# Optimization experiments

Hardware: AMD Instinct MI355X
Metric: run time of the kernel (lower is better)

Reference implementation:

```python
import jax, jax.numpy as jnp
import numpy as np

NV, NC, E, H, L = 100_000, 420_000, 630_000, 128, 8
ALPHA, THETA = 0.1, 0.5


def _seg_mean(msgs, dst, n_dst):
    # mean aggregation over destination segments (PyG SAGEConv default)
    s = jax.ops.segment_sum(msgs, dst, num_segments=n_dst)
    cnt = jax.ops.segment_sum(jnp.ones((dst.shape[0], 1), msgs.dtype), dst, num_segments=n_dst)
    return s / jnp.maximum(cnt, 1.0)


def _sage(x_src, x_dst, src, dst, n_dst, Wl, bl, Wr):
    # SAGEConv: lin_l(mean_{j in N(i)} x_j) + lin_r(x_i); lin_r has no bias
    agg = _seg_mean(x_src[src], dst, n_dst)
    return agg @ Wl + bl + x_dst @ Wr


def setup_inputs() -> dict:
    key = jax.random.key(0)
    ks = jax.random.split(key, 40)
    k = iter(range(40))
    rn = lambda shape, s=0.05: jax.random.normal(ks[next(k)], shape, jnp.float32) * s
    inp = {}
    inp['x_variable'] = jax.random.normal(ks[next(k)], (NV, 4), jnp.float32)
    inp['x_clause'] = jax.random.normal(ks[next(k)], (NC, 1), jnp.float32)
    src_p = jax.random.randint(ks[next(k)], (E,), 0, NV)
    dst_p = jax.random.randint(ks[next(k)], (E,), 0, NC)
    src_n = jax.random.randint(ks[next(k)], (E,), 0, NV)
    dst_n = jax.random.randint(ks[next(k)], (E,), 0, NC)
    inp['edge_pos'] = jnp.stack([src_p, dst_p])  # variable -> clause
    inp['edge_neg'] = jnp.stack([src_n, dst_n])
    inp['W_vemb'] = rn((4, H)); inp['b_vemb'] = rn((H,))
    inp['W_cemb'] = rn((1, H)); inp['b_cemb'] = rn((H,))
    for tag in ('pos', 'neg', 'rpos', 'rneg'):
        inp[f'Wl_{tag}'] = rn((L, H, H)); inp[f'bl_{tag}'] = rn((L, H))
        inp[f'Wr_{tag}'] = rn((L, H, H))
    inp['Wv'] = rn((L, H, H)); inp['bv'] = rn((L, H))
    inp['W_fin'] = rn((H, 1)); inp['b_fin'] = rn((1,))
    return inp


def reference(x_variable, x_clause, edge_pos, edge_neg,
              W_vemb, b_vemb, W_cemb, b_cemb,
              Wl_pos, bl_pos, Wr_pos, Wl_neg, bl_neg, Wr_neg,
              Wl_rpos, bl_rpos, Wr_rpos, Wl_rneg, bl_rneg, Wr_rneg,
              Wv, bv, W_fin, b_fin):
    v_h0 = jax.nn.relu(x_variable @ W_vemb + b_vemb)
    c_h0 = jax.nn.relu(x_clause @ W_cemb + b_cemb)
    v_h, c_h = v_h0, c_h0
    sp, dp = edge_pos[0], edge_pos[1]
    sn, dn = edge_neg[0], edge_neg[1]
    for i in range(L):
        v_old = v_h
        # HeteroConv(aggr='sum'): clause gets pos_in + neg_in, variable gets rev_pos_in + rev_neg_in
        c_new = (_sage(v_h, c_h, sp, dp, NC, Wl_pos[i], bl_pos[i], Wr_pos[i]) +
                 _sage(v_h, c_h, sn, dn, NC, Wl_neg[i], bl_neg[i], Wr_neg[i]))
        v_new = (_sage(c_h, v_h, dp, sp, NV, Wl_rpos[i], bl_rpos[i], Wr_rpos[i]) +
                 _sage(c_h, v_h, dn, sn, NV, Wl_rneg[i], bl_rneg[i], Wr_rneg[i]))
        v_h = (1.0 - ALPHA) * v_new + ALPHA * v_h0
        c_h = (1.0 - ALPHA) * c_new + ALPHA * c_h0
        beta = float(np.log(THETA / (i + 1) + 1.0))
        v_h = (1.0 - beta) * v_h + beta * (v_h @ Wv[i] + bv[i])
        v_h = v_h + v_old  # use_inter_layer_res=True
        v_h, c_h = jax.nn.relu(v_h), jax.nn.relu(c_h)
    return v_h @ W_fin + b_fin
```

## Files before the change

### kernel.cpp

```cpp
#include <hip/hip_runtime.h>
#include <math.h>

#define NVV 100000
#define NCC 420000
#define EE  630000
#define HH  128
#define LL  8

typedef unsigned int uint;
typedef unsigned short ushort;
typedef __attribute__((ext_vector_type(8))) short bf16x8;
typedef __attribute__((ext_vector_type(4))) float f32x4;

#define MFMA16(a,b,c) __builtin_amdgcn_mfma_f32_16x16x32_bf16(a,b,c,0,0,0)
#define SW(r,k) (((r)<<7) + ((k) ^ (((r)&7)<<3)))

__device__ inline float bf2f(uint u){ return __uint_as_float(u << 16); }
__device__ inline uint  f2bf(float f){
  uint b = __float_as_uint(f);
  return (b + 0x7FFFu + ((b >> 16) & 1u)) >> 16;
}
__device__ inline uint pack2(float a, float b){ return f2bf(a) | (f2bf(b) << 16); }
__device__ inline float4 relu4(float4 v){
  v.x = fmaxf(v.x, 0.f); v.y = fmaxf(v.y, 0.f);
  v.z = fmaxf(v.z, 0.f); v.w = fmaxf(v.w, 0.f);
  return v;
}

__global__ void k_sentinel(float* out, float v){
  if (blockIdx.x == 0 && threadIdx.x == 0) out[0] = v;
}

__device__ inline float4 vemb4(const float* __restrict__ xv, const float* __restrict__ W,
                               const float* __restrict__ b, int i, int h4){
  float x0 = xv[4*i+0], x1 = xv[4*i+1], x2 = xv[4*i+2], x3 = xv[4*i+3];
  float4 w0 = *(const float4*)(W + 0*HH + h4);
  float4 w1 = *(const float4*)(W + 1*HH + h4);
  float4 w2 = *(const float4*)(W + 2*HH + h4);
  float4 w3 = *(const float4*)(W + 3*HH + h4);
  float4 bb = *(const float4*)(b + h4);
  float4 r;
  r.x = fmaf(x0,w0.x, fmaf(x1,w1.x, fmaf(x2,w2.x, fmaf(x3,w3.x, bb.x))));
  r.y = fmaf(x0,w0.y, fmaf(x1,w1.y, fmaf(x2,w2.y, fmaf(x3,w3.y, bb.y))));
  r.z = fmaf(x0,w0.z, fmaf(x1,w1.z, fmaf(x2,w2.z, fmaf(x3,w3.z, bb.z))));
  r.w = fmaf(x0,w0.w, fmaf(x1,w1.w, fmaf(x2,w2.w, fmaf(x3,w3.w, bb.w))));
  return r;
}

__global__ void k_embed_v(const float* __restrict__ xv, const float* __restrict__ W,
                          const float* __restrict__ b, float* __restrict__ out){
  int tid = blockIdx.x * 256 + threadIdx.x;
  int i = tid >> 5;
  if (i >= NVV) return;
  int h4 = (tid & 31) << 2;
  *(float4*)(out + (size_t)i*HH + h4) = relu4(vemb4(xv, W, b, i, h4));
}

__global__ void k_embed_c(const float* __restrict__ xc, const float* __restrict__ W,
                          const float* __restrict__ b, uint* __restrict__ out){
  int tid = blockIdx.x * 256 + threadIdx.x;
  int i = tid >> 5;
  if (i >= NCC) return;
  int c2 = tid & 31;
  int h4 = c2 << 2;
  float x0 = xc[i];
  float4 w = *(const float4*)(W + h4);
  float4 bb = *(const float4*)(b + h4);
  float4 r;
  r.x = fmaxf(fmaf(x0, w.x, bb.x), 0.f);
  r.y = fmaxf(fmaf(x0, w.y, bb.y), 0.f);
  r.z = fmaxf(fmaf(x0, w.z, bb.z), 0.f);
  r.w = fmaxf(fmaf(x0, w.w, bb.w), 0.f);
  uint2 o; o.x = pack2(r.x, r.y); o.y = pack2(r.z, r.w);
  *(uint2*)(out + (size_t)i*64 + c2*2) = o;
}

__global__ void k_prep(const float* __restrict__ Wl_pos, const float* __restrict__ Wl_neg,
                       const float* __restrict__ Wl_rpos, const float* __restrict__ Wl_rneg,
                       const float* __restrict__ Wv, const float* __restrict__ Wr_pos,
                       const float* __restrict__ Wr_neg, const float* __restrict__ Wr_rpos,
                       const float* __restrict__ Wr_rneg, ushort* __restrict__ wt){
  int tid = blockIdx.x * 256 + threadIdx.x;
  int n4 = tid & 31, k = (tid >> 5) & 127, l = (tid >> 12) & 7, m = tid >> 15;
  const float* s1; const float* s2 = nullptr;
  switch (m){
    case 0: s1 = Wl_pos;  break;
    case 1: s1 = Wl_neg;  break;
    case 2: s1 = Wl_rpos; break;
    case 3: s1 = Wl_rneg; break;
    case 4: s1 = Wv;      break;
    case 5: s1 = Wr_pos;  s2 = Wr_neg;  break;
    default: s1 = Wr_rpos; s2 = Wr_rneg; break;
  }
  size_t o = (size_t)l*16384 + (size_t)k*128 + n4*4;
  float4 w = *(const float4*)(s1 + o);
  if (s2){
    float4 w2 = *(const float4*)(s2 + o);
    w.x += w2.x; w.y += w2.y; w.z += w2.z; w.w += w2.w;
  }
  ushort* hi = wt + (size_t)((m*LL + l)*2    )*16384;
  ushort* lo = wt + (size_t)((m*LL + l)*2 + 1)*16384;
  float vv[4] = {w.x, w.y, w.z, w.w};
  #pragma unroll
  for (int e = 0; e < 4; ++e){
    int n = n4*4 + e;
    uint h = f2bf(vv[e]);
    float r = vv[e] - bf2f(h);
    hi[SW(n, k)] = (ushort)h;
    lo[SW(n, k)] = (ushort)f2bf(r);
  }
}

__global__ void k_counti(const int* __restrict__ d, int* cnt, int n){
  int i = blockIdx.x * 256 + threadIdx.x;
  if (i < n) atomicAdd(&cnt[d[i]], 1);
}

#define SCAN256(ts, t) \
  for (int off = 1; off < 256; off <<= 1){ \
    int _a = (t >= off) ? ts[t - off] : 0; \
    __syncthreads(); \
    ts[t] += _a; \
    __syncthreads(); \
  }

__global__ void k_scanb(const int* __restrict__ in, int* __restrict__ out,
                        int* __restrict__ part, int n){
  __shared__ int ts[256];
  int b = blockIdx.x, t = threadIdx.x;
  int base = b*1024 + t*4;
  int v0 = (base+0 < n) ? in[base+0] : 0;
  int v1 = (base+1 < n) ? in[base+1] : 0;
  int v2 = (base+2 < n) ? in[base+2] : 0;
  int v3 = (base+3 < n) ? in[base+3] : 0;
  int s1 = v0, s2 = s1+v1, s3 = s2+v2, tsum = s3+v3;
  ts[t] = tsum; __syncthreads();
  SCAN256(ts, t)
  int excl = ts[t] - tsum;
  if (base+0 < n) out[base+0] = excl;
  if (base+1 < n) out[base+1] = excl + s1;
  if (base+2 < n) out[base+2] = excl + s2;
  if (base+3 < n) out[base+3] = excl + s3;
  if (t == 255) part[b] = ts[255];
}

__global__ void k_scanp(int* p, int nb){
  __shared__ int ts[256];
  __shared__ int carry;
  int t = threadIdx.x;
  if (t == 0) carry = 0;
  __syncthreads();
  for (int c = 0; c*256 < nb; ++c){
    int i = c*256 + t;
    int v = (i < nb) ? p[i] : 0;
    ts[t] = v; __syncthreads();
    SCAN256(ts, t)
    int excl = ts[t] - v + carry;
    if (i < nb) p[i] = excl;
    int tot = ts[255];
    __syncthreads();
    if (t == 0) carry += tot;
    __syncthreads();
  }
}

__global__ void k_scana(int* out, const int* __restrict__ part, int n){
  int i = blockIdx.x * 256 + threadIdx.x;
  if (i < n) out[i] += part[i >> 10];
}

__global__ void k_fill(const int* __restrict__ dst, const int* __restrict__ pay,
                       int* cur, int* __restrict__ eo, int n){
  int i = blockIdx.x * 256 + threadIdx.x;
  if (i >= n) return;
  int p = atomicAdd(&cur[dst[i]], 1);
  eo[p] = pay[i];
}

__global__ void k_vgather(const uint* __restrict__ ch,
                          const int* __restrict__ ipp, const int* __restrict__ epp,
                          const int* __restrict__ ipn, const int* __restrict__ epn,
                          uint* __restrict__ Up, uint* __restrict__ Un){
  int g = blockIdx.x * 256 + threadIdx.x;
  int v = g >> 6, lane = g & 63;
  if (v >= NVV) return;
  int sp = v ? ipp[v-1] : 0, ePos = ipp[v];
  int sn = v ? ipn[v-1] : 0, eNeg = ipn[v];
  float p0 = 0.f, p1 = 0.f, n0 = 0.f, n1 = 0.f;
  int jp = sp, jn = sn;
  while (jp < ePos && jn < eNeg){
    uint up = ch[(size_t)epp[jp]*64 + lane];
    uint un = ch[(size_t)epn[jn]*64 + lane];
    p0 += bf2f(up & 0xFFFFu); p1 += bf2f(up >> 16);
    n0 += bf2f(un & 0xFFFFu); n1 += bf2f(un >> 16);
    ++jp; ++jn;
  }
  for (; jp < ePos; ++jp){
    uint up = ch[(size_t)epp[jp]*64 + lane];
    p0 += bf2f(up & 0xFFFFu); p1 += bf2f(up >> 16);
  }
  for (; jn < eNeg; ++jn){
    uint un = ch[(size_t)epn[jn]*64 + lane];
    n0 += bf2f(un & 0xFFFFu); n1 += bf2f(un >> 16);
  }
  float ivp = 1.f / fmaxf((float)(ePos - sp), 1.f);
  float ivn = 1.f / fmaxf((float)(eNeg - sn), 1.f);
  Up[(size_t)v*64 + lane] = pack2(p0*ivp, p1*ivp);
  Un[(size_t)v*64 + lane] = pack2(n0*ivn, n1*ivn);
}

__device__ inline void stA_bf16(const uint4* __restrict__ A, ushort* As, int m0, int M, int t){
  #pragma unroll
  for (int j = 0; j < 4; ++j){
    int idx = j*512 + t, r = idx >> 4, c = idx & 15;
    uint4 v = make_uint4(0,0,0,0);
    if (m0 + r < M) v = A[(size_t)(m0 + r)*16 + c];
    *(uint4*)(As + SW(r, c*8)) = v;
  }
}

__device__ inline void stA_f32(const float* __restrict__ A, ushort* As, int m0, int M, int t){
  const float4* A4 = (const float4*)A;
  #pragma unroll
  for (int j = 0; j < 8; ++j){
    int idx = j*512 + t, r = idx >> 5, c = idx & 31;
    float4 v = make_float4(0.f,0.f,0.f,0.f);
    if (m0 + r < M) v = A4[(size_t)(m0 + r)*32 + c];
    uint2 u; u.x = pack2(v.x, v.y); u.y = pack2(v.z, v.w);
    *(uint2*)(As + SW(r, c*4)) = u;
  }
}

__device__ inline void stB(const uint4* __restrict__ Bt, ushort* Bs, int t){
  #pragma unroll
  for (int j = 0; j < 4; ++j) ((uint4*)Bs)[j*512 + t] = Bt[j*512 + t];
}

__device__ inline void kloop(const ushort* As, const ushort* Bs, int wr, int wc,
                             int l15, int g, f32x4 acc[2][4]){
  #pragma unroll
  for (int kk = 0; kk < 4; ++kk){
    int kb = kk*32 + g*8;
    bf16x8 a0 = *(const bf16x8*)(As + SW(wr*32 + l15,      kb));
    bf16x8 a1 = *(const bf16x8*)(As + SW(wr*32 + 16 + l15, kb));
    #pragma unroll
    for (int ni = 0; ni < 4; ++ni){
      int n = wc*64 + ni*16 + l15;
      bf16x8 b = *(const bf16x8*)(Bs + SW(n, kb));
      acc[0][ni] = MFMA16(a0, b, acc[0][ni]);
      acc[1][ni] = MFMA16(a1, b, acc[1][ni]);
    }
  }
}

__device__ inline void accStoreF(float* ldsF, f32x4 acc[2][4], int wr, int wc, int l15, int g){
  #pragma unroll
  for (int mi = 0; mi < 2; ++mi)
    #pragma unroll
    for (int ni = 0; ni < 4; ++ni)
      #pragma unroll
      for (int j = 0; j < 4; ++j)
        ldsF[(wr*32 + mi*16 + g*4 + j)*128 + wc*64 + ni*16 + l15] = acc[mi][ni][j];
}

__device__ inline void accStoreFsw(float* ldsF, f32x4 acc[2][4], int wr, int wc, int l15, int g){
  #pragma unroll
  for (int mi = 0; mi < 2; ++mi)
    #pragma unroll
    for (int ni = 0; ni < 4; ++ni)
      #pragma unroll
      for (int j = 0; j < 4; ++j){
        int r = wr*32 + mi*16 + g*4 + j;
        int c = wc*64 + ni*16 + l15;
        ldsF[r*128 + (((c >> 2) ^ (r & 31)) << 2) + (c & 3)] = acc[mi][ni][j];
      }
}

__device__ inline void accStoreBf(ushort* dst, f32x4 acc[2][4], int wr, int wc, int l15, int g){
  #pragma unroll
  for (int mi = 0; mi < 2; ++mi)
    #pragma unroll
    for (int ni = 0; ni < 4; ++ni)
      #pragma unroll
      for (int j = 0; j < 4; ++j)
        dst[(wr*32 + mi*16 + g*4 + j)*128 + wc*64 + ni*16 + l15] =
            (ushort)f2bf(acc[mi][ni][j]);
}

#define MMHEAD \
  __shared__ ushort lds[32768]; \
  ushort* As = lds; ushort* Bs = lds + 16384; \
  float* accumF = (float*)lds; \
  int t = threadIdx.x, m0 = blockIdx.x * 128; \
  int w = t >> 6, l = t & 63, wr = w >> 1, wc = w & 1, l15 = l & 15, g = l >> 4; \
  const f32x4 zz = {0.f, 0.f, 0.f, 0.f}; \
  (void)accumF;

#define ZACC(A) { \
  _Pragma("unroll") for (int mi_ = 0; mi_ < 2; ++mi_) \
    _Pragma("unroll") for (int ni_ = 0; ni_ < 4; ++ni_) A[mi_][ni_] = zz; }

__global__ __launch_bounds__(512) void k_fused_v(
    const uint4* __restrict__ AggP, const uint4* __restrict__ AggN,
    const uint4* __restrict__ Bph, const uint4* __restrict__ Bpl,
    const uint4* __restrict__ Bnh, const uint4* __restrict__ Bnl,
    const uint4* __restrict__ Bfh, const uint4* __restrict__ Bfl,
    const uint4* __restrict__ Byph, const uint4* __restrict__ Bypl,
    const uint4* __restrict__ Bynh, const uint4* __restrict__ Bynl,
    const uint4* __restrict__ Bvh, const uint4* __restrict__ Bvl,
    const float* __restrict__ xv, const float* __restrict__ Wve, const float* __restrict__ bve,
    const float* __restrict__ blp, const float* __restrict__ bln, const float* __restrict__ bvv,
    float omb, float beta,
    uint4* __restrict__ Yp, uint4* __restrict__ Yn, float* vh, int M){
  MMHEAD
  f32x4 accM[2][4], accP[2][4], accN[2][4];
  ZACC(accM) ZACC(accP) ZACC(accN)

  stA_bf16(AggP, As, m0, M, t); stB(Bph, Bs, t); __syncthreads();
  kloop(As, Bs, wr, wc, l15, g, accM); __syncthreads();
  stB(Bpl, Bs, t); __syncthreads();
  kloop(As, Bs, wr, wc, l15, g, accM); __syncthreads();
  stA_bf16(AggN, As, m0, M, t); stB(Bnh, Bs, t); __syncthreads();
  kloop(As, Bs, wr, wc, l15, g, accM); __syncthreads();
  stB(Bnl, Bs, t); __syncthreads();
  kloop(As, Bs, wr, wc, l15, g, accM); __syncthreads();
  stA_f32(vh, As, m0, M, t); stB(Bfh, Bs, t); __syncthreads();
  kloop(As, Bs, wr, wc, l15, g, accM); __syncthreads();
  stB(Bfl, Bs, t); __syncthreads();
  kloop(As, Bs, wr, wc, l15, g, accM); __syncthreads();
  stB(Byph, Bs, t); __syncthreads();
  kloop(As, Bs, wr, wc, l15, g, accP); __syncthreads();
  stB(Bypl, Bs, t); __syncthreads();
  kloop(As, Bs, wr, wc, l15, g, accP); __syncthreads();
  stB(Bynh, Bs, t); __syncthreads();
  kloop(As, Bs, wr, wc, l15, g, accN); __syncthreads();
  stB(Bynl, Bs, t); __syncthreads();
  kloop(As, Bs, wr, wc, l15, g, accN); __syncthreads();

  accStoreBf(lds,         accP, wr, wc, l15, g);
  accStoreBf(lds + 16384, accN, wr, wc, l15, g);
  __syncthreads();
  #pragma unroll
  for (int j = 0; j < 4; ++j){
    int idx = j*512 + t, r = idx >> 4, c = idx & 15;
    if (m0 + r < M){
      Yp[(size_t)(m0 + r)*16 + c] = ((const uint4*)lds)[idx];
      Yn[(size_t)(m0 + r)*16 + c] = ((const uint4*)(lds + 16384))[idx];
    }
  }
  __syncthreads();

  accStoreF(accumF, accM, wr, wc, l15, g);
  __syncthreads();
  float4 vreg[8];
  #pragma unroll
  for (int j = 0; j < 8; ++j){
    int idx = j*512 + t, r = idx >> 5, c4 = idx & 31;
    int row = m0 + r;
    float4 o = make_float4(0.f,0.f,0.f,0.f);
    if (row < M){
      float4 a4 = ((const float4*)accumF)[r*32 + c4];
      float4 bp = ((const float4*)blp)[c4];
      float4 bn = ((const float4*)bln)[c4];
      float4 h = relu4(vemb4(xv, Wve, bve, row, c4*4));
      o.x = 0.9f*(a4.x + bp.x + bn.x) + 0.1f*h.x;
      o.y = 0.9f*(a4.y + bp.y + bn.y) + 0.1f*h.y;
      o.z = 0.9f*(a4.z + bp.z + bn.z) + 0.1f*h.z;
      o.w = 0.9f*(a4.w + bp.w + bn.w) + 0.1f*h.w;
    }
    vreg[j] = o;
  }
  __syncthreads();
  #pragma unroll
  for (int j = 0; j < 8; ++j){
    int idx = j*512 + t, r = idx >> 5, c4 = idx & 31;
    uint2 u; u.x = pack2(vreg[j].x, vreg[j].y); u.y = pack2(vreg[j].z, vreg[j].w);
    *(uint2*)(As + SW(r, c4*4)) = u;
  }
  f32x4 accT[2][4];
  ZACC(accT)
  stB(Bvh, Bs, t); __syncthreads();
  kloop(As, Bs, wr, wc, l15, g, accT); __syncthreads();
  stB(Bvl, Bs, t); __syncthreads();
  kloop(As, Bs, wr, wc, l15, g, accT);

  float* ldsH = (float*)Bs;
  #pragma unroll
  for (int half = 0; half < 2; ++half){
    __syncthreads();
    if ((wr >> 1) == half){
      int rbase = (wr & 1)*32;
      #pragma unroll
      for (int mi = 0; mi < 2; ++mi)
        #pragma unroll
        for (int ni = 0; ni < 4; ++ni)
          #pragma unroll
          for (int j = 0; j < 4; ++j)
            ldsH[(rbase + mi*16 + g*4 + j)*128 + wc*64 + ni*16 + l15] = accT[mi][ni][j];
    }
    __syncthreads();
    #pragma unroll
    for (int j = 0; j < 4; ++j){
      int idx = j*512 + t, r2 = idx >> 5, c4 = idx & 31;
      int row = m0 + half*64 + r2;
      if (row >= M) continue;
      float4 a4 = ((const float4*)ldsH)[r2*32 + c4];
      uint2 um = *(const uint2*)(As + SW(half*64 + r2, c4*4));
      float4 bb = ((const float4*)bvv)[c4];
      float4 vo = *(const float4*)(vh + (size_t)row*HH + c4*4);
      float m0f = bf2f(um.x & 0xFFFFu), m1f = bf2f(um.x >> 16);
      float m2f = bf2f(um.y & 0xFFFFu), m3f = bf2f(um.y >> 16);
      float4 o;
      o.x = fmaxf(omb*m0f + beta*(a4.x + bb.x) + vo.x, 0.f);
      o.y = fmaxf(omb*m1f + beta*(a4.y + bb.y) + vo.y, 0.f);
      o.z = fmaxf(omb*m2f + beta*(a4.z + bb.z) + vo.z, 0.f);
      o.w = fmaxf(omb*m3f + beta*(a4.w + bb.w) + vo.w, 0.f);
      *(float4*)(vh + (size_t)row*HH + c4*4) = o;
    }
  }
}

__device__ inline void addrow8(float f[8], uint4 u){
  f[0] += bf2f(u.x & 0xFFFFu); f[1] += bf2f(u.x >> 16);
  f[2] += bf2f(u.y & 0xFFFFu); f[3] += bf2f(u.y >> 16);
  f[4] += bf2f(u.z & 0xFFFFu); f[5] += bf2f(u.z >> 16);
  f[6] += bf2f(u.w & 0xFFFFu); f[7] += bf2f(u.w >> 16);
}

__global__ __launch_bounds__(512) void k_mm_c(const uint4* ch,
    const uint4* __restrict__ Bh, const uint4* __restrict__ Bl,
    const int* __restrict__ ipp, const int* __restrict__ ecp,
    const int* __restrict__ ipn, const int* __restrict__ ecn,
    const uint4* __restrict__ Yp, const uint4* __restrict__ Yn,
    const float* __restrict__ xc, const float* __restrict__ Wc, const float* __restrict__ bc,
    const float* __restrict__ blp, const float* __restrict__ bln,
    uint4* chout){
  MMHEAD
  f32x4 acc[2][4];
  ZACC(acc)
  stA_bf16(ch, As, m0, NCC, t); stB(Bh, Bs, t); __syncthreads();
  kloop(As, Bs, wr, wc, l15, g, acc); __syncthreads();
  stB(Bl, Bs, t); __syncthreads();
  kloop(As, Bs, wr, wc, l15, g, acc); __syncthreads();
  accStoreFsw(accumF, acc, wr, wc, l15, g);
  __syncthreads();

  int c16 = t & 15;
  int rg  = t >> 4;
  #pragma unroll
  for (int pass = 0; pass < 4; ++pass){
    int r = pass*32 + rg;
    int row = m0 + r;
    if (row >= NCC) continue;
    float fp[8] = {0,0,0,0,0,0,0,0};
    float fn[8] = {0,0,0,0,0,0,0,0};
    int sp = row ? ipp[row-1] : 0, ePos = ipp[row];
    int sn = row ? ipn[row-1] : 0, eNeg = ipn[row];
    int jp = sp, jn = sn;
    while (jp < ePos && jn < eNeg){
      uint4 up = Yp[(size_t)ecp[jp]*16 + c16];
      uint4 un = Yn[(size_t)ecn[jn]*16 + c16];
      addrow8(fp, up);
      addrow8(fn, un);
      ++jp; ++jn;
    }
    for (; jp < ePos; ++jp) addrow8(fp, Yp[(size_t)ecp[jp]*16 + c16]);
    for (; jn < eNeg; ++jn) addrow8(fn, Yn[(size_t)ecn[jn]*16 + c16]);
    float invp = 1.f / fmaxf((float)(ePos - sp), 1.f);
    float invn = 1.f / fmaxf((float)(eNeg - sn), 1.f);

    int gi0 = c16*2, gi1 = gi0 + 1;
    float4 res0 = ((const float4*)accumF)[r*32 + (gi0 ^ (r & 31))];
    float4 res1 = ((const float4*)accumF)[r*32 + (gi1 ^ (r & 31))];
    float4 wc0 = ((const float4*)Wc)[gi0],  wc1 = ((const float4*)Wc)[gi1];
    float4 bc0 = ((const float4*)bc)[gi0],  bc1 = ((const float4*)bc)[gi1];
    float4 bp0 = ((const float4*)blp)[gi0], bp1 = ((const float4*)blp)[gi1];
    float4 bn0 = ((const float4*)bln)[gi0], bn1 = ((const float4*)bln)[gi1];
    float xcv = xc[row];
    float res[8] = {res0.x,res0.y,res0.z,res0.w, res1.x,res1.y,res1.z,res1.w};
    float wcv[8] = {wc0.x,wc0.y,wc0.z,wc0.w, wc1.x,wc1.y,wc1.z,wc1.w};
    float bcv[8] = {bc0.x,bc0.y,bc0.z,bc0.w, bc1.x,bc1.y,bc1.z,bc1.w};
    float bpv[8] = {bp0.x,bp0.y,bp0.z,bp0.w, bp1.x,bp1.y,bp1.z,bp1.w};
    float bnv[8] = {bn0.x,bn0.y,bn0.z,bn0.w, bn1.x,bn1.y,bn1.z,bn1.w};
    float o[8];
    #pragma unroll
    for (int k = 0; k < 8; ++k){
      float h = fmaxf(fmaf(xcv, wcv[k], bcv[k]), 0.f);
      float m = fmaf(fp[k], invp, fn[k]*invn);
      o[k] = fmaxf(0.9f*(m + res[k] + bpv[k] + bnv[k]) + 0.1f*h, 0.f);
    }
    uint4 u;
    u.x = pack2(o[0], o[1]); u.y = pack2(o[2], o[3]);
    u.z = pack2(o[4], o[5]); u.w = pack2(o[6], o[7]);
    chout[(size_t)row*16 + c16] = u;
  }
}

__global__ void k_final(const float* __restrict__ vh, const float* __restrict__ wf,
                        const float* __restrict__ bf, float* __restrict__ out){
  int wid = (blockIdx.x * 256 + threadIdx.x) >> 6;
  if (wid >= NVV) return;
  int lane = threadIdx.x & 63;
  float2 a = *(const float2*)(vh + (size_t)wid*HH + lane*2);
  float2 w = *(const float2*)(wf + lane*2);
  float s = a.x*w.x + a.y*w.y;
  #pragma unroll
  for (int off = 32; off > 0; off >>= 1) s += __shfl_down(s, off);
  if (lane == 0) out[wid] = s + bf[0];
}

extern "C" void kernel_launch(void* const* d_in, const int* in_sizes, int n_in,
                              void* d_out, int out_size, void* d_ws, size_t ws_size,
                              hipStream_t stream) {
  const float* xv  = (const float*)d_in[0];
  const float* xc  = (const float*)d_in[1];
  const int*   ep  = (const int*)d_in[2];
  const int*   en  = (const int*)d_in[3];
  const float* Wve = (const float*)d_in[4];
  const float* bve = (const float*)d_in[5];
  const float* Wce = (const float*)d_in[6];
  const float* bce = (const float*)d_in[7];
  const float* Wl_pos  = (const float*)d_in[8];
  const float* bl_pos  = (const float*)d_in[9];
  const float* Wr_pos  = (const float*)d_in[10];
  const float* Wl_neg  = (const float*)d_in[11];
  const float* bl_neg  = (const float*)d_in[12];
  const float* Wr_neg  = (const float*)d_in[13];
  const float* Wl_rpos = (const float*)d_in[14];
  const float* bl_rpos = (const float*)d_in[15];
  const float* Wr_rpos = (const float*)d_in[16];
  const float* Wl_rneg = (const float*)d_in[17];
  const float* bl_rneg = (const float*)d_in[18];
  const float* Wr_rneg = (const float*)d_in[19];
  const float* Wv  = (const float*)d_in[20];
  const float* bv  = (const float*)d_in[21];
  const float* Wf  = (const float*)d_in[22];
  const float* bf  = (const float*)d_in[23];
  float* out = (float*)d_out;

  size_t off = 0;
  auto alloc = [&](size_t bytes) -> void* {
    void* p = (char*)d_ws + off;
    off = (off + bytes + 255) & ~(size_t)255;
    return p;
  };
  uint*   c_h  = (uint*)  alloc((size_t)NCC*64*sizeof(uint));
  float*  v_h  = (float*) alloc((size_t)NVV*HH*sizeof(float));
  uint*   U1   = (uint*)  alloc((size_t)NVV*64*sizeof(uint));
  uint*   U2   = (uint*)  alloc((size_t)NVV*64*sizeof(uint));
  ushort* wt   = (ushort*)alloc((size_t)7*LL*2*16384*sizeof(ushort));
  int*   ipc_p = (int*)  alloc((size_t)NCC*sizeof(int));
  int*   ec_p  = (int*)  alloc((size_t)EE*sizeof(int));
  int*   ipc_n = (int*)  alloc((size_t)NCC*sizeof(int));
  int*   ec_n  = (int*)  alloc((size_t)EE*sizeof(int));
  int*   ipv_p = (int*)  alloc((size_t)NVV*sizeof(int));
  int*   ev_p  = (int*)  alloc((size_t)EE*sizeof(int));
  int*   ipv_n = (int*)  alloc((size_t)NVV*sizeof(int));
  int*   ev_n  = (int*)  alloc((size_t)EE*sizeof(int));
  int*   part  = (int*)  alloc(4096);
  if (off > ws_size){
    k_sentinel<<<1, 64, 0, stream>>>(out, (float)(ws_size >> 20));
    return;
  }

  const int TB = 256;
  const int gE  = (EE + TB-1)/TB;
  const int gV  = (NVV*32 + TB-1)/TB;
  const int gC  = (NCC*32 + TB-1)/TB;
  const int gGv = (NVV + 127)/128;
  const int gGc = (NCC + 127)/128;
  const int gWd = (NVV*64 + TB-1)/TB;

  auto wp = [&](int m, int l, int h) -> const uint4* {
    return (const uint4*)(wt + (size_t)((m*LL + l)*2 + h)*16384);
  };

  auto build = [&](const int* dst, const int* pay, int nd, int* ip, int* eo){
    hipMemsetAsync(ip, 0, (size_t)nd*sizeof(int), stream);
    k_counti<<<gE, TB, 0, stream>>>(dst, ip, EE);
    int nb = (nd + 1023)/1024;
    k_scanb<<<nb, TB, 0, stream>>>(ip, ip, part, nd);
    k_scanp<<<1, TB, 0, stream>>>(part, nb);
    k_scana<<<(nd + TB-1)/TB, TB, 0, stream>>>(ip, part, nd);
    k_fill<<<gE, TB, 0, stream>>>(dst, pay, ip, eo, EE);
  };
  build(ep + EE, ep,      NCC, ipc_p, ec_p);
  build(en + EE, en,      NCC, ipc_n, ec_n);
  build(ep,      ep + EE, NVV, ipv_p, ev_p);
  build(en,      en + EE, NVV, ipv_n, ev_n);

  k_prep<<<(7*LL*128*32)/TB, TB, 0, stream>>>(Wl_pos, Wl_neg, Wl_rpos, Wl_rneg, Wv,
                                              Wr_pos, Wr_neg, Wr_rpos, Wr_rneg, wt);

  k_embed_v<<<gV, TB, 0, stream>>>(xv, Wve, bve, v_h);
  k_embed_c<<<gC, TB, 0, stream>>>(xc, Wce, bce, c_h);

  for (int l = 0; l < LL; ++l){
    const size_t bo = (size_t)l*HH;
    double beta_d = log(0.5/(double)(l+1) + 1.0);

    k_vgather<<<gWd, TB, 0, stream>>>(c_h, ipv_p, ev_p, ipv_n, ev_n, U1, U2);
    k_fused_v<<<gGv, 512, 0, stream>>>((const uint4*)U1, (const uint4*)U2,
                                       wp(2,l,0), wp(2,l,1), wp(3,l,0), wp(3,l,1),
                                       wp(6,l,0), wp(6,l,1),
                                       wp(0,l,0), wp(0,l,1), wp(1,l,0), wp(1,l,1),
                                       wp(4,l,0), wp(4,l,1),
                                       xv, Wve, bve, bl_rpos + bo, bl_rneg + bo, bv + bo,
                                       (float)(1.0 - beta_d), (float)beta_d,
                                       (uint4*)U1, (uint4*)U2, v_h, NVV);
    k_mm_c<<<gGc, 512, 0, stream>>>((const uint4*)c_h, wp(5,l,0), wp(5,l,1),
                                    ipc_p, ec_p, ipc_n, ec_n,
                                    (const uint4*)U1, (const uint4*)U2,
                                    xc, Wce, bce, bl_pos + bo, bl_neg + bo,
                                    (uint4*)c_h);
  }

  k_final<<<gWd, TB, 0, stream>>>(v_h, Wf, bf, out);
}
```

Measured before the change: 3.517 ms.

## Prefetch B tiles into registers and batch neighbor gathers for memory-level parallelism

```diff
diff --git a/kernel.cpp b/kernel.cpp
--- a/kernel.cpp
+++ b/kernel.cpp
@@ -186,25 +186,58 @@
   if (v >= NVV) return;
   int sp = v ? ipp[v-1] : 0, ePos = ipp[v];
   int sn = v ? ipn[v-1] : 0, eNeg = ipn[v];
-  float p0 = 0.f, p1 = 0.f, n0 = 0.f, n1 = 0.f;
-  int jp = sp, jn = sn;
-  while (jp < ePos && jn < eNeg){
-    uint up = ch[(size_t)epp[jp]*64 + lane];
-    uint un = ch[(size_t)epn[jn]*64 + lane];
-    p0 += bf2f(up & 0xFFFFu); p1 += bf2f(up >> 16);
-    n0 += bf2f(un & 0xFFFFu); n1 += bf2f(un >> 16);
-    ++jp; ++jn;
-  }
-  for (; jp < ePos; ++jp){
-    uint up = ch[(size_t)epp[jp]*64 + lane];
-    p0 += bf2f(up & 0xFFFFu); p1 += bf2f(up >> 16);
-  }
-  for (; jn < eNeg; ++jn){
-    uint un = ch[(size_t)epn[jn]*64 + lane];
-    n0 += bf2f(un & 0xFFFFu); n1 += bf2f(un >> 16);
-  }
-  float ivp = 1.f / fmaxf((float)(ePos - sp), 1.f);
-  float ivn = 1.f / fmaxf((float)(eNeg - sn), 1.f);
+  int dp = ePos - sp, dn = eNeg - sn;
+  int a0 = dp>0 ? epp[sp+0] : 0, a1 = dp>1 ? epp[sp+1] : 0;
+  int a2 = dp>2 ? epp[sp+2] : 0, a3 = dp>3 ? epp[sp+3] : 0;
+  int a4 = dp>4 ? epp[sp+4] : 0, a5 = dp>5 ? epp[sp+5] : 0;
+  int a6 = dp>6 ? epp[sp+6] : 0, a7 = dp>7 ? epp[sp+7] : 0;
+  int b0 = dn>0 ? epn[sn+0] : 0, b1 = dn>1 ? epn[sn+1] : 0;
+  int b2 = dn>2 ? epn[sn+2] : 0, b3 = dn>3 ? epn[sn+3] : 0;
+  int b4 = dn>4 ? epn[sn+4] : 0, b5 = dn>5 ? epn[sn+5] : 0;
+  int b6 = dn>6 ? epn[sn+6] : 0, b7 = dn>7 ? epn[sn+7] : 0;
+  uint ua0 = dp>0 ? ch[(size_t)a0*64 + lane] : 0;
+  uint ua1 = dp>1 ? ch[(size_t)a1*64 + lane] : 0;
+  uint ua2 = dp>2 ? ch[(size_t)a2*64 + lane] : 0;
+  uint ua3 = dp>3 ? ch[(size_t)a3*64 + lane] : 0;
+  uint ua4 = dp>4 ? ch[(size_t)a4*64 + lane] : 0;
+  uint ua5 = dp>5 ? ch[(size_t)a5*64 + lane] : 0;
+  uint ua6 = dp>6 ? ch[(size_t)a6*64 + lane] : 0;
+  uint ua7 = dp>7 ? ch[(size_t)a7*64 + lane] : 0;
+  uint ub0 = dn>0 ? ch[(size_t)b0*64 + lane] : 0;
+  uint ub1 = dn>1 ? ch[(size_t)b1*64 + lane] : 0;
+  uint ub2 = dn>2 ? ch[(size_t)b2*64 + lane] : 0;
+  uint ub3 = dn>3 ? ch[(size_t)b3*64 + lane] : 0;
+  uint ub4 = dn>4 ? ch[(size_t)b4*64 + lane] : 0;
+  uint ub5 = dn>5 ? ch[(size_t)b5*64 + lane] : 0;
+  uint ub6 = dn>6 ? ch[(size_t)b6*64 + lane] : 0;
+  uint ub7 = dn>7 ? ch[(size_t)b7*64 + lane] : 0;
+  float p0, p1, n0, n1;
+  p0  = bf2f(ua0 & 0xFFFFu); p1  = bf2f(ua0 >> 16);
+  p0 += bf2f(ua1 & 0xFFFFu); p1 += bf2f(ua1 >> 16);
+  p0 += bf2f(ua2 & 0xFFFFu); p1 += bf2f(ua2 >> 16);
+  p0 += bf2f(ua3 & 0xFFFFu); p1 += bf2f(ua3 >> 16);
+  p0 += bf2f(ua4 & 0xFFFFu); p1 += bf2f(ua4 >> 16);
+  p0 += bf2f(ua5 & 0xFFFFu); p1 += bf2f(ua5 >> 16);
+  p0 += bf2f(ua6 & 0xFFFFu); p1 += bf2f(ua6 >> 16);
+  p0 += bf2f(ua7 & 0xFFFFu); p1 += bf2f(ua7 >> 16);
+  n0  = bf2f(ub0 & 0xFFFFu); n1  = bf2f(ub0 >> 16);
+  n0 += bf2f(ub1 & 0xFFFFu); n1 += bf2f(ub1 >> 16);
+  n0 += bf2f(ub2 & 0xFFFFu); n1 += bf2f(ub2 >> 16);
+  n0 += bf2f(ub3 & 0xFFFFu); n1 += bf2f(ub3 >> 16);
+  n0 += bf2f(ub4 & 0xFFFFu); n1 += bf2f(ub4 >> 16);
+  n0 += bf2f(ub5 & 0xFFFFu); n1 += bf2f(ub5 >> 16);
+  n0 += bf2f(ub6 & 0xFFFFu); n1 += bf2f(ub6 >> 16);
+  n0 += bf2f(ub7 & 0xFFFFu); n1 += bf2f(ub7 >> 16);
+  for (int j = sp + 8; j < ePos; ++j){
+    uint u = ch[(size_t)epp[j]*64 + lane];
+    p0 += bf2f(u & 0xFFFFu); p1 += bf2f(u >> 16);
+  }
+  for (int j = sn + 8; j < eNeg; ++j){
+    uint u = ch[(size_t)epn[j]*64 + lane];
+    n0 += bf2f(u & 0xFFFFu); n1 += bf2f(u >> 16);
+  }
+  float ivp = 1.f / fmaxf((float)dp, 1.f);
+  float ivn = 1.f / fmaxf((float)dn, 1.f);
   Up[(size_t)v*64 + lane] = pack2(p0*ivp, p1*ivp);
   Un[(size_t)v*64 + lane] = pack2(n0*ivn, n1*ivn);
 }
@@ -229,6 +262,30 @@
     uint2 u; u.x = pack2(v.x, v.y); u.y = pack2(v.z, v.w);
     *(uint2*)(As + SW(r, c*4)) = u;
   }
+}
+
+__device__ inline void ldA_bf16(const uint4* __restrict__ A, uint4 ar[4], int m0, int M, int t){
+  #pragma unroll
+  for (int j = 0; j < 4; ++j){
+    int idx = j*512 + t, r = idx >> 4, c = idx & 15;
+    ar[j] = make_uint4(0,0,0,0);
+    if (m0 + r < M) ar[j] = A[(size_t)(m0 + r)*16 + c];
+  }
+}
+__device__ inline void wrA(const uint4 ar[4], ushort* As, int t){
+  #pragma unroll
+  for (int j = 0; j < 4; ++j){
+    int idx = j*512 + t, r = idx >> 4, c = idx & 15;
+    *(uint4*)(As + SW(r, c*8)) = ar[j];
+  }
+}
+__device__ inline void ldB(const uint4* __restrict__ Bt, uint4 br[4], int t){
+  #pragma unroll
+  for (int j = 0; j < 4; ++j) br[j] = Bt[j*512 + t];
+}
+__device__ inline void wrB(ushort* Bs, const uint4 br[4], int t){
+  #pragma unroll
+  for (int j = 0; j < 4; ++j) ((uint4*)Bs)[j*512 + t] = br[j];
 }
 
 __device__ inline void stB(const uint4* __restrict__ Bt, ushort* Bs, int t){
@@ -315,28 +372,43 @@
   MMHEAD
   f32x4 accM[2][4], accP[2][4], accN[2][4];
   ZACC(accM) ZACC(accP) ZACC(accN)
-
-  stA_bf16(AggP, As, m0, M, t); stB(Bph, Bs, t); __syncthreads();
+  uint4 br[4], ar[4];
+
+  ldB(Bph, br, t);
+  stA_bf16(AggP, As, m0, M, t);
+  wrB(Bs, br, t);
+  __syncthreads();
+  ldB(Bpl, br, t);
   kloop(As, Bs, wr, wc, l15, g, accM); __syncthreads();
-  stB(Bpl, Bs, t); __syncthreads();
+  wrB(Bs, br, t); __syncthreads();
+  ldB(Bnh, br, t); ldA_bf16(AggN, ar, m0, M, t);
   kloop(As, Bs, wr, wc, l15, g, accM); __syncthreads();
-  stA_bf16(AggN, As, m0, M, t); stB(Bnh, Bs, t); __syncthreads();
+  wrB(Bs, br, t); wrA(ar, As, t); __syncthreads();
+  ldB(Bnl, br, t);
   kloop(As, Bs, wr, wc, l15, g, accM); __syncthreads();
-  stB(Bnl, Bs, t); __syncthreads();
+  wrB(Bs, br, t); __syncthreads();
+  ldB(Bfh, br, t);
   kloop(As, Bs, wr, wc, l15, g, accM); __syncthreads();
-  stA_f32(vh, As, m0, M, t); stB(Bfh, Bs, t); __syncthreads();
+  wrB(Bs, br, t); stA_f32(vh, As, m0, M, t); __syncthreads();
+  ldB(Bfl, br, t);
   kloop(As, Bs, wr, wc, l15, g, accM); __syncthreads();
-  stB(Bfl, Bs, t); __syncthreads();
+  wrB(Bs, br, t); __syncthreads();
+  ldB(Byph, br, t);
   kloop(As, Bs, wr, wc, l15, g, accM); __syncthreads();
-  stB(Byph, Bs, t); __syncthreads();
+  wrB(Bs, br, t); __syncthreads();
+  ldB(Bypl, br, t);
   kloop(As, Bs, wr, wc, l15, g, accP); __syncthreads();
-  stB(Bypl, Bs, t); __syncthreads();
+  wrB(Bs, br, t); __syncthreads();
+  ldB(Bynh, br, t);
   kloop(As, Bs, wr, wc, l15, g, accP); __syncthreads();
-  stB(Bynh, Bs, t); __syncthreads();
+  wrB(Bs, br, t); __syncthreads();
+  ldB(Bynl, br, t);
   kloop(As, Bs, wr, wc, l15, g, accN); __syncthreads();
-  stB(Bynl, Bs, t); __syncthreads();
-  kloop(As, Bs, wr, wc, l15, g, accN); __syncthreads();
-
+  wrB(Bs, br, t); __syncthreads();
+  ldB(Bvh, br, t);
+  kloop(As, Bs, wr, wc, l15, g, accN);
+
+  __syncthreads();
   accStoreBf(lds,         accP, wr, wc, l15, g);
   accStoreBf(lds + 16384, accN, wr, wc, l15, g);
   __syncthreads();
@@ -377,11 +449,13 @@
     uint2 u; u.x = pack2(vreg[j].x, vreg[j].y); u.y = pack2(vreg[j].z, vreg[j].w);
     *(uint2*)(As + SW(r, c4*4)) = u;
   }
+  wrB(Bs, br, t);
+  __syncthreads();
+  ldB(Bvl, br, t);
   f32x4 accT[2][4];
   ZACC(accT)
-  stB(Bvh, Bs, t); __syncthreads();
   kloop(As, Bs, wr, wc, l15, g, accT); __syncthreads();
-  stB(Bvl, Bs, t); __syncthreads();
+  wrB(Bs, br, t); __syncthreads();
   kloop(As, Bs, wr, wc, l15, g, accT);
 
   float* ldsH = (float*)Bs;
@@ -447,27 +521,35 @@
 
   int c16 = t & 15;
   int rg  = t >> 4;
+  const uint4 z4 = make_uint4(0,0,0,0);
   #pragma unroll
   for (int pass = 0; pass < 4; ++pass){
     int r = pass*32 + rg;
     int row = m0 + r;
     if (row >= NCC) continue;
+    int sp = row ? ipp[row-1] : 0, ePos = ipp[row];
+    int sn = row ? ipn[row-1] : 0, eNeg = ipn[row];
+    int dp = ePos - sp, dn = eNeg - sn;
+    int ia0 = dp>0 ? ecp[sp+0] : 0, ia1 = dp>1 ? ecp[sp+1] : 0;
+    int ia2 = dp>2 ? ecp[sp+2] : 0, ia3 = dp>3 ? ecp[sp+3] : 0;
+    int ib0 = dn>0 ? ecn[sn+0] : 0, ib1 = dn>1 ? ecn[sn+1] : 0;
+    int ib2 = dn>2 ? ecn[sn+2] : 0, ib3 = dn>3 ? ecn[sn+3] : 0;
+    uint4 ra0 = dp>0 ? Yp[(size_t)ia0*16 + c16] : z4;
+    uint4 ra1 = dp>1 ? Yp[(size_t)ia1*16 + c16] : z4;
+    uint4 ra2 = dp>2 ? Yp[(size_t)ia2*16 + c16] : z4;
+    uint4 ra3 = dp>3 ? Yp[(size_t)ia3*16 + c16] : z4;
+    uint4 rb0 = dn>0 ? Yn[(size_t)ib0*16 + c16] : z4;
+    uint4 rb1 = dn>1 ? Yn[(size_t)ib1*16 + c16] : z4;
+    uint4 rb2 = dn>2 ? Yn[(size_t)ib2*16 + c16] : z4;
+    uint4 rb3 = dn>3 ? Yn[(size_t)ib3*16 + c16] : z4;
     float fp[8] = {0,0,0,0,0,0,0,0};
     float fn[8] = {0,0,0,0,0,0,0,0};
-    int sp = row ? ipp[row-1] : 0, ePos = ipp[row];
-    int sn = row ? ipn[row-1] : 0, eNeg = ipn[row];
-    int jp = sp, jn = sn;
-    while (jp < ePos && jn < eNeg){
-      uint4 up = Yp[(size_t)ecp[jp]*16 + c16];
-      uint4 un = Yn[(size_t)ecn[jn]*16 + c16];
-      addrow8(fp, up);
-      addrow8(fn, un);
-      ++jp; ++jn;
-    }
-    for (; jp < ePos; ++jp) addrow8(fp, Yp[(size_t)ecp[jp]*16 + c16]);
-    for (; jn < eNeg; ++jn) addrow8(fn, Yn[(size_t)ecn[jn]*16 + c16]);
-    float invp = 1.f / fmaxf((float)(ePos - sp), 1.f);
-    float invn = 1.f / fmaxf((float)(eNeg - sn), 1.f);
+    addrow8(fp, ra0); addrow8(fp, ra1); addrow8(fp, ra2); addrow8(fp, ra3);
+    addrow8(fn, rb0); addrow8(fn, rb1); addrow8(fn, rb2); addrow8(fn, rb3);
+    for (int j = sp + 4; j < ePos; ++j) addrow8(fp, Yp[(size_t)ecp[j]*16 + c16]);
+    for (int j = sn + 4; j < eNeg; ++j) addrow8(fn, Yn[(size_t)ecn[j]*16 + c16]);
+    float invp = 1.f / fmaxf((float)dp, 1.f);
+    float invn = 1.f / fmaxf((float)dn, 1.f);
 
     int gi0 = c16*2, gi1 = gi0 + 1;
     float4 res0 = ((const float4*)accumF)[r*32 + (gi0 ^ (r & 31))];
```

Result: slower. 4.003 ms (+13.8%).
